# Optimization experiments

Measured on AMD Instinct MI355X. Metric: run time of the kernel, lower is better.

Reference implementation:

```python
import jax, jax.numpy as jnp
import numpy as np

KS = 3
K3 = KS ** 3
NUM_K = 4
KM_ITERS = 10  # fixed Lloyd iterations (original runs to tolerance)


def _unfold3d(xp, d, h, w):
    # xp: [B, C, d+2, h+2, w+2] -> [B, C, d, h, w, 27]; kernel dims flattened as (k1,k2,k3)
    sl = [xp[:, :, i:i + d, j:j + h, l:l + w]
          for i in range(KS) for j in range(KS) for l in range(KS)]
    return jnp.stack(sl, axis=-1)


def _kmeans(pts):
    # pts: [N, C]. Deterministic init with first NUM_K points, fixed Lloyd iterations.
    cent0 = pts[:NUM_K]

    def assign(cent):
        d2 = (jnp.sum(pts * pts, -1, keepdims=True)
              - 2.0 * (pts @ cent.T) + jnp.sum(cent * cent, -1))  # [N, K]
        return jnp.argmin(d2, axis=-1)

    def step(cent, _):
        oh = jax.nn.one_hot(assign(cent), NUM_K, dtype=pts.dtype)  # [N, K]
        cnt = jnp.maximum(oh.sum(0), 1.0)
        cent = (oh.T @ pts) / cnt[:, None]
        return cent, None

    cent, _ = jax.lax.scan(step, cent0, None, length=KM_ITERS)
    return assign(cent), cent


def _mlp3(z, w1, b1, w2, b2, w3, b3):
    z = jax.nn.relu(z @ w1 + b1)
    z = jax.nn.relu(z @ w2 + b2)
    return z @ w3 + b3


def reference(x, proj_w, base_w, gk_w1, gk_b1, gk_w2, gk_b2, gk_w3, gk_b3,
              gb_w1, gb_b1, gb_w2, gb_b2, gb_w3, gb_b3, prelu_a):
    b, c, d, h, w = x.shape
    o = base_w.shape[0]
    n = d * h * w
    x_in = x
    # 1x1x1 input projection (no bias)
    xp = jnp.einsum('oi,bidhw->bodhw', proj_w, x)
    xp = jnp.pad(xp, ((0, 0), (0, 0), (1, 1), (1, 1), (1, 1)))
    patches = _unfold3d(xp, d, h, w)                                # [b,c,d,h,w,27]
    # mean_type 's': mean over kernel dims -> per-voxel channel summary
    x_mean = patches.mean(-1).reshape(b, c, n).transpose(0, 2, 1)   # [b,n,c]
    idx, cent = jax.vmap(_kmeans)(x_mean)                           # [b,n], [b,K,c]
    feat = cent.reshape(b, NUM_K * c)
    # per-cluster dynamic kernel gates in (0,1)
    w_i = jax.nn.sigmoid(_mlp3(feat, gk_w1, gk_b1, gk_w2, gk_b2, gk_w3, gk_b3))
    w_i = w_i.reshape(b, NUM_K, K3).transpose(1, 0, 2)[:, :, None, None, :]  # [K,b,1,1,27]
    weight = (w_i * base_w).reshape(NUM_K, b, o, c * K3)            # [K,b,o,c*27]
    bias = _mlp3(feat, gb_w1, gb_b1, gb_w2, gb_b2, gb_w3, gb_b3)
    bias = bias.reshape(b, NUM_K, o).transpose(1, 0, 2)[..., None]  # [K,b,o,1]
    # im2col: [b, c*27, n] with (c, k) channel-major flattening as in the torch rearrange
    xf = patches.reshape(b, c, n, K3).transpose(0, 1, 3, 2).reshape(b, c * K3, n)
    out = jnp.einsum('kbof,bfn->kbon', weight, xf) + bias           # [K,b,o,n]
    mask = jax.nn.one_hot(idx, NUM_K, dtype=out.dtype)              # [b,n,K]
    out = (out * mask.transpose(2, 0, 1)[:, :, None, :]).sum(0)     # [b,o,n]
    out = out.reshape(b, o, d, h, w)
    out = jnp.where(out >= 0, out, prelu_a * out)                   # PReLU (single param)
    return out + x_in


def setup_inputs():
    key = jax.random.key(0)
    ks = jax.random.split(key, 12)
    B, C, O, D = 1, 64, 64, 40
    inner, inner2 = 128, 64
    fin = C * NUM_K

    def lin(k, i, o_):
        s = 1.0 / np.sqrt(i)
        return jax.random.uniform(k, (i, o_), jnp.float32, -s, s)

    return {
        'x': jax.random.normal(ks[0], (B, C, D, D, D), jnp.float32),
        'proj_w': jax.random.normal(ks[1], (C, C), jnp.float32) / np.sqrt(C),
        'base_w': jax.random.normal(ks[2], (O, C, K3), jnp.float32) / np.sqrt(C * K3),
        'gk_w1': lin(ks[3], fin, inner), 'gk_b1': jnp.zeros((inner,), jnp.float32),
        'gk_w2': lin(ks[4], inner, inner), 'gk_b2': jnp.zeros((inner,), jnp.float32),
        'gk_w3': lin(ks[5], inner, K3 * NUM_K), 'gk_b3': jnp.zeros((K3 * NUM_K,), jnp.float32),
        'gb_w1': lin(ks[6], fin, inner2), 'gb_b1': jnp.zeros((inner2,), jnp.float32),
        'gb_w2': lin(ks[7], inner2, inner2), 'gb_b2': jnp.zeros((inner2,), jnp.float32),
        'gb_w3': lin(ks[8], inner2, O * NUM_K), 'gb_b3': jnp.zeros((O * NUM_K,), jnp.float32),
        'prelu_a': jnp.full((1,), 0.25, jnp.float32),
    }
```

## Files before the change

### kernel.cpp

```cpp
#include <hip/hip_runtime.h>
#include <math.h>

typedef short v8s __attribute__((ext_vector_type(8)));
typedef float v4f __attribute__((ext_vector_type(4)));

#define NVOX 64000
#define NPAD 74088
#define P2   1764
#define GSTR 592704
#define NCPY 32
#define ITST (NCPY*260)

__device__ __forceinline__ unsigned short bf16rne(float f){
  unsigned int u = __float_as_uint(f);
  u += 0x7FFFu + ((u >> 16) & 1u);
  return (unsigned short)(u >> 16);
}

__global__ __launch_bounds__(256) void prep_k(const float* __restrict__ x,
                                              const float* __restrict__ pw,
                                              float* __restrict__ xp,
                                              short* __restrict__ xpt,
                                              const float* __restrict__ bw,
                                              short* __restrict__ bwb,
                                              float* __restrict__ km){
  int tid = threadIdx.x;
  int bid = blockIdx.x;
  if (bid < 1000){
    int m = (bid >> 2) * 256 + tid;
    int quarter = bid & 3;
    float xv[64];
#pragma unroll
    for (int i = 0; i < 64; i++) xv[i] = x[(size_t)i * NVOX + m];
    int d = m / 1600; int r = m - d * 1600; int h = r / 40; int w = r - h * 40;
    int p = ((d + 1) * 42 + (h + 1)) * 42 + (w + 1);
    const float4* pw4 = (const float4*)pw;
    for (int g8 = quarter * 2; g8 < quarter * 2 + 2; g8++){
      v8s pk;
#pragma unroll
      for (int j = 0; j < 8; j++){
        int co = g8 * 8 + j;
        float acc = 0.f;
#pragma unroll
        for (int q = 0; q < 16; q++){
          float4 pv = pw4[co * 16 + q];
          acc = fmaf(pv.x, xv[4*q+0], acc);
          acc = fmaf(pv.y, xv[4*q+1], acc);
          acc = fmaf(pv.z, xv[4*q+2], acc);
          acc = fmaf(pv.w, xv[4*q+3], acc);
        }
        xp[(size_t)co * NVOX + m] = acc;
        pk[j] = (short)bf16rne(acc);
      }
      *(v8s*)(xpt + (size_t)g8 * GSTR + (size_t)p * 8) = pk;
    }
  } else if (bid < 1432){
    int e = (bid - 1000) * 256 + tid;
    int t5 = e >> 12; int rem = e & 4095;
    int o = rem >> 6; int c = rem & 63;
    bwb[e] = (short)bf16rne(bw[(o * 64 + c) * 27 + t5]);
  } else if (bid < 1472){
    v8s z = (v8s){0,0,0,0,0,0,0,0};
    for (int p = (bid - 1432) * 256 + tid; p < NPAD; p += 40 * 256){
      int d = p / P2; int rem = p - d * P2; int h = rem / 42; int w = rem - h * 42;
      if (d == 0 || d == 41 || h == 0 || h == 41 || w == 0 || w == 41){
#pragma unroll
        for (int g = 0; g < 8; g++)
          *(v8s*)(xpt + (size_t)g * GSTR + (size_t)p * 8) = z;
      }
    }
  } else {
    for (int j = (bid - 1472) * 256 + tid; j < 10 * ITST; j += 82 * 256)
      km[j] = 0.f;
  }
}

__global__ __launch_bounds__(256) void boxwh_k(const float* __restrict__ in,
                                               float* __restrict__ out){
  __shared__ float s0[1600], s1[1600];
  size_t base = (size_t)blockIdx.x * 1600;
  int t = threadIdx.x;
  for (int e = t; e < 1600; e += 256) s0[e] = in[base + e];
  __syncthreads();
  for (int e = t; e < 1600; e += 256){
    int w = e % 40;
    float s = s0[e];
    if (w > 0)  s += s0[e - 1];
    if (w < 39) s += s0[e + 1];
    s1[e] = s;
  }
  __syncthreads();
  for (int e = t; e < 1600; e += 256){
    int h = e / 40;
    float s = s1[e];
    if (h > 0)  s += s1[e - 40];
    if (h < 39) s += s1[e + 40];
    out[base + e] = s;
  }
}

__global__ __launch_bounds__(256) void boxdt_k(const float* __restrict__ in,
                                               float* __restrict__ out,
                                               float* __restrict__ acc1){
  __shared__ float tile[64][65];
  __shared__ float s_cent[256];
  __shared__ float s_cc[4];
  __shared__ float s_red[260];
  __shared__ int   s_kb[64];
  int t = threadIdx.x;
  int nb = blockIdx.x * 64;
  int l = t & 63, g = t >> 6;
  {
    int k = t >> 6, c = t & 63;
    s_cent[t] = (in[(size_t)c * NVOX + k] + in[(size_t)c * NVOX + k + 1600]) * (1.f / 27.f);
  }
  for (int j = t; j < 260; j += 256) s_red[j] = 0.f;
  int n = nb + l;
  int d = n / 1600;
  for (int cc = g; cc < 64; cc += 4){
    const float* b = in + (size_t)cc * NVOX + n;
    float s = b[0];
    if (d > 0)  s += b[-1600];
    if (d < 39) s += b[1600];
    tile[cc][l] = s * (1.f / 27.f);
  }
  __syncthreads();
  if (t < 4){
    float s = 0.f;
    for (int c = 0; c < 64; c++){ float v = s_cent[t * 64 + c]; s = fmaf(v, v, s); }
    s_cc[t] = s;
  }
  __syncthreads();
  if (t < 64){
    float d0 = 0.f, d1 = 0.f, d2 = 0.f, d3 = 0.f;
    for (int c = 0; c < 64; c++){
      float v = tile[c][t];
      d0 = fmaf(s_cent[c], v, d0);
      d1 = fmaf(s_cent[64 + c], v, d1);
      d2 = fmaf(s_cent[128 + c], v, d2);
      d3 = fmaf(s_cent[192 + c], v, d3);
    }
    float sc0 = s_cc[0] - 2.f * d0;
    float sc1 = s_cc[1] - 2.f * d1;
    float sc2 = s_cc[2] - 2.f * d2;
    float sc3 = s_cc[3] - 2.f * d3;
    int kb = 0; float bs = sc0;
    if (sc1 < bs){ bs = sc1; kb = 1; }
    if (sc2 < bs){ bs = sc2; kb = 2; }
    if (sc3 < bs){ bs = sc3; kb = 3; }
    s_kb[t] = kb;
  }
  __syncthreads();
  {
    int lane = t & 63, wv = t >> 6;
    float a0 = 0.f, a1 = 0.f, a2 = 0.f, a3 = 0.f;
#pragma unroll
    for (int j = 0; j < 16; j++){
      int p = wv * 16 + j;
      float v = tile[lane][p];
      int kj = s_kb[p];
      a0 += (kj == 0) ? v : 0.f;
      a1 += (kj == 1) ? v : 0.f;
      a2 += (kj == 2) ? v : 0.f;
      a3 += (kj == 3) ? v : 0.f;
    }
    atomicAdd(&s_red[lane], a0);
    atomicAdd(&s_red[64 + lane], a1);
    atomicAdd(&s_red[128 + lane], a2);
    atomicAdd(&s_red[192 + lane], a3);
  }
  if (t < 4){
    float c = 0.f;
    for (int p = 0; p < 64; p++) c += (s_kb[p] == t) ? 1.f : 0.f;
    s_red[256 + t] = c;
  }
  __syncthreads();
  float* kslot = acc1 + (blockIdx.x & (NCPY - 1)) * 260;
  for (int j = t; j < 260; j += 256) atomicAdd(&kslot[j], s_red[j]);
  for (int nn = g; nn < 64; nn += 4)
    out[(size_t)(nb + nn) * 64 + l] = tile[l][nn];
}

__global__ __launch_bounds__(256) void assign_k(const float* __restrict__ xmt,
                                                const float* __restrict__ kin,
                                                float* __restrict__ kout,
                                                int* __restrict__ idx, int mode,
                      const float* __restrict__ w1, const float* __restrict__ b1,
                      const float* __restrict__ w2, const float* __restrict__ b2,
                      const float* __restrict__ w3, const float* __restrict__ b3,
                      const float* __restrict__ u1, const float* __restrict__ c1,
                      const float* __restrict__ u2, const float* __restrict__ c2,
                      const float* __restrict__ u3, const float* __restrict__ c3,
                      float* __restrict__ wi, float* __restrict__ bias){
  __shared__ float s_cent[256];
  __shared__ float s_cc[4];
  __shared__ float s_red[260];
  __shared__ float s_x[256 * 65];
  __shared__ int   s_kb[256];
  __shared__ float s_h1[128], s_h2[128], s_g1[64], s_g2[64];
  int t = threadIdx.x, lane = t & 63, wv = t >> 6;
  int n = blockIdx.x * 256 + t;
  {
    float sum = 0.f, cnt = 0.f;
#pragma unroll
    for (int s = 0; s < NCPY; s++){
      sum += kin[s * 260 + t];
      cnt += kin[s * 260 + 256 + (t >> 6)];
    }
    s_cent[t] = sum / fmaxf(cnt, 1.f);
  }
  for (int j = t; j < 260; j += 256) s_red[j] = 0.f;
  __syncthreads();
  if (t < 4){
    const float4* cc4 = (const float4*)(s_cent + t * 64);
    float s = 0.f;
#pragma unroll
    for (int q = 0; q < 16; q++){
      float4 v = cc4[q];
      s = fmaf(v.x, v.x, s); s = fmaf(v.y, v.y, s);
      s = fmaf(v.z, v.z, s); s = fmaf(v.w, v.w, s);
    }
    s_cc[t] = s;
  }
  __syncthreads();
  const float4* xt = (const float4*)(xmt + (size_t)n * 64);
  float4 xq[16];
#pragma unroll
  for (int q = 0; q < 16; q++) xq[q] = xt[q];
  float d0 = 0.f, d1 = 0.f, d2 = 0.f, d3 = 0.f;
  const float4* c4 = (const float4*)s_cent;
#pragma unroll
  for (int q = 0; q < 16; q++){
    float4 p0 = c4[q], p1 = c4[16 + q], p2 = c4[32 + q], p3 = c4[48 + q];
    d0 = fmaf(p0.x, xq[q].x, d0); d0 = fmaf(p0.y, xq[q].y, d0);
    d0 = fmaf(p0.z, xq[q].z, d0); d0 = fmaf(p0.w, xq[q].w, d0);
    d1 = fmaf(p1.x, xq[q].x, d1); d1 = fmaf(p1.y, xq[q].y, d1);
    d1 = fmaf(p1.z, xq[q].z, d1); d1 = fmaf(p1.w, xq[q].w, d1);
    d2 = fmaf(p2.x, xq[q].x, d2); d2 = fmaf(p2.y, xq[q].y, d2);
    d2 = fmaf(p2.z, xq[q].z, d2); d2 = fmaf(p2.w, xq[q].w, d2);
    d3 = fmaf(p3.x, xq[q].x, d3); d3 = fmaf(p3.y, xq[q].y, d3);
    d3 = fmaf(p3.z, xq[q].z, d3); d3 = fmaf(p3.w, xq[q].w, d3);
  }
  float sc0 = s_cc[0] - 2.f * d0;
  float sc1 = s_cc[1] - 2.f * d1;
  float sc2 = s_cc[2] - 2.f * d2;
  float sc3 = s_cc[3] - 2.f * d3;
  int kb = 0; float bs = sc0;
  if (sc1 < bs){ bs = sc1; kb = 1; }
  if (sc2 < bs){ bs = sc2; kb = 2; }
  if (sc3 < bs){ bs = sc3; kb = 3; }
  if (mode){
    idx[n] = kb;
    if (blockIdx.x == 0){
      __syncthreads();
      if (t < 128){
        float z = b1[t];
        for (int i = 0; i < 256; i++) z = fmaf(s_cent[i], w1[i * 128 + t], z);
        s_h1[t] = fmaxf(z, 0.f);
      }
      if (t < 64){
        float z = c1[t];
        for (int i = 0; i < 256; i++) z = fmaf(s_cent[i], u1[i * 64 + t], z);
        s_g1[t] = fmaxf(z, 0.f);
      }
      __syncthreads();
      if (t < 128){
        float z = b2[t];
        for (int i = 0; i < 128; i++) z = fmaf(s_h1[i], w2[i * 128 + t], z);
        s_h2[t] = fmaxf(z, 0.f);
      }
      if (t < 64){
        float z = c2[t];
        for (int i = 0; i < 64; i++) z = fmaf(s_g1[i], u2[i * 64 + t], z);
        s_g2[t] = fmaxf(z, 0.f);
      }
      __syncthreads();
      if (t < 108){
        float z = b3[t];
        for (int i = 0; i < 128; i++) z = fmaf(s_h2[i], w3[i * 108 + t], z);
        wi[t] = 1.f / (1.f + expf(-z));
      }
      {
        float z = c3[t];
        for (int i = 0; i < 64; i++) z = fmaf(s_g2[i], u3[i * 256 + t], z);
        bias[t] = z;
      }
    }
    return;
  }
  s_kb[t] = kb;
#pragma unroll
  for (int q = 0; q < 16; q++){
    s_x[t * 65 + 4*q + 0] = xq[q].x;
    s_x[t * 65 + 4*q + 1] = xq[q].y;
    s_x[t * 65 + 4*q + 2] = xq[q].z;
    s_x[t * 65 + 4*q + 3] = xq[q].w;
  }
  __syncthreads();
  float a0 = 0.f, a1 = 0.f, a2 = 0.f, a3 = 0.f;
  int rowbase = wv * 64;
#pragma unroll 16
  for (int j = 0; j < 64; j++){
    float v = s_x[(rowbase + j) * 65 + lane];
    int kj = s_kb[rowbase + j];
    a0 += (kj == 0) ? v : 0.f;
    a1 += (kj == 1) ? v : 0.f;
    a2 += (kj == 2) ? v : 0.f;
    a3 += (kj == 3) ? v : 0.f;
  }
  atomicAdd(&s_red[lane], a0);
  atomicAdd(&s_red[64 + lane], a1);
  atomicAdd(&s_red[128 + lane], a2);
  atomicAdd(&s_red[192 + lane], a3);
#pragma unroll
  for (int kk = 0; kk < 4; kk++){
    unsigned long long m = __ballot(kb == kk);
    if (lane == 0) atomicAdd(&s_red[256 + kk], (float)__popcll(m));
  }
  __syncthreads();
  float* kslot = kout + (blockIdx.x & (NCPY - 1)) * 260;
  for (int j = t; j < 260; j += 256) atomicAdd(&kslot[j], s_red[j]);
}

__global__ __launch_bounds__(256) void conv_k(const short* __restrict__ xpt,
                                              const short* __restrict__ bwb,
                                              const float* __restrict__ wi,
                                              const float* __restrict__ bias,
                                              const int* __restrict__ idx,
                                              const float* __restrict__ x,
                                              const float* __restrict__ pa,
                                              float* __restrict__ out){
  static const int POFF[27] = {
    -P2-42-1, -P2-42, -P2-42+1, -P2-1, -P2, -P2+1, -P2+42-1, -P2+42, -P2+42+1,
    -42-1, -42, -42+1, -1, 0, 1, 42-1, 42, 42+1,
    P2-42-1, P2-42, P2-42+1, P2-1, P2, P2+1, P2+42-1, P2+42, P2+42+1 };
  __shared__ float s_wi[108];
  __shared__ float s_bias[256];
  __shared__ float s_acc[64 * 68];
  int tid = threadIdx.x;
  for (int j = tid; j < 108; j += 256) s_wi[j] = wi[j];
  s_bias[tid] = bias[tid];
  __syncthreads();
  int wv = tid >> 6, lane = tid & 63;
  int kc = wv & 1, mh = wv >> 1;
  int col = lane & 15, kg = lane >> 4;
  int vb = blockIdx.x * 64;
  int p4[4], ki4[4];
#pragma unroll
  for (int nt = 0; nt < 4; nt++){
    int v = vb + nt * 16 + col;
    ki4[nt] = idx[v];
    int d = v / 1600; int r = v - d * 1600; int h = r / 40; int w = r - h * 40;
    p4[nt] = ((d + 1) * 42 + (h + 1)) * 42 + (w + 1);
  }
  const short* bg = xpt + (size_t)(kc * 4 + kg) * GSTR;
  const short* bp0 = bg + (size_t)p4[0] * 8;
  const short* bp1 = bg + (size_t)p4[1] * 8;
  const short* bp2 = bg + (size_t)p4[2] * 8;
  const short* bp3 = bg + (size_t)p4[3] * 8;
  int ao0 = (mh * 32 + col) * 64 + kc * 32 + kg * 8;
  int ao1 = ao0 + 16 * 64;
  v4f acc[2][4];
#pragma unroll
  for (int m2 = 0; m2 < 2; m2++)
#pragma unroll
    for (int nt = 0; nt < 4; nt++) acc[m2][nt] = (v4f){0.f, 0.f, 0.f, 0.f};
  v4f zero = {0.f, 0.f, 0.f, 0.f};
#pragma unroll 9
  for (int t = 0; t < 27; t++){
    int po8 = POFF[t] * 8;
    v8s a0 = *(const v8s*)(bwb + t * 4096 + ao0);
    v8s a1 = *(const v8s*)(bwb + t * 4096 + ao1);
    v8s b0 = *(const v8s*)(bp0 + po8);
    v8s b1 = *(const v8s*)(bp1 + po8);
    v8s b2 = *(const v8s*)(bp2 + po8);
    v8s b3 = *(const v8s*)(bp3 + po8);
    float wk0 = s_wi[ki4[0] * 27 + t];
    float wk1 = s_wi[ki4[1] * 27 + t];
    float wk2 = s_wi[ki4[2] * 27 + t];
    float wk3 = s_wi[ki4[3] * 27 + t];
    v4f tp;
    tp = __builtin_amdgcn_mfma_f32_16x16x32_bf16(a0, b0, zero, 0, 0, 0); acc[0][0] += tp * wk0;
    tp = __builtin_amdgcn_mfma_f32_16x16x32_bf16(a1, b0, zero, 0, 0, 0); acc[1][0] += tp * wk0;
    tp = __builtin_amdgcn_mfma_f32_16x16x32_bf16(a0, b1, zero, 0, 0, 0); acc[0][1] += tp * wk1;
    tp = __builtin_amdgcn_mfma_f32_16x16x32_bf16(a1, b1, zero, 0, 0, 0); acc[1][1] += tp * wk1;
    tp = __builtin_amdgcn_mfma_f32_16x16x32_bf16(a0, b2, zero, 0, 0, 0); acc[0][2] += tp * wk2;
    tp = __builtin_amdgcn_mfma_f32_16x16x32_bf16(a1, b2, zero, 0, 0, 0); acc[1][2] += tp * wk2;
    tp = __builtin_amdgcn_mfma_f32_16x16x32_bf16(a0, b3, zero, 0, 0, 0); acc[0][3] += tp * wk3;
    tp = __builtin_amdgcn_mfma_f32_16x16x32_bf16(a1, b3, zero, 0, 0, 0); acc[1][3] += tp * wk3;
  }
  __syncthreads();
  if (kc == 1){
#pragma unroll
    for (int m2 = 0; m2 < 2; m2++)
#pragma unroll
      for (int nt = 0; nt < 4; nt++)
        *(v4f*)(&s_acc[(nt * 16 + col) * 68 + mh * 32 + m2 * 16 + kg * 4]) = acc[m2][nt];
  }
  __syncthreads();
  if (kc == 0){
    float pav = pa[0];
#pragma unroll
    for (int m2 = 0; m2 < 2; m2++){
#pragma unroll
      for (int nt = 0; nt < 4; nt++){
        v4f other = *(const v4f*)(&s_acc[(nt * 16 + col) * 68 + mh * 32 + m2 * 16 + kg * 4]);
        v4f sum = acc[m2][nt] + other;
        int n = vb + nt * 16 + col;
#pragma unroll
        for (int r = 0; r < 4; r++){
          int o = mh * 32 + m2 * 16 + kg * 4 + r;
          float val = sum[r] + s_bias[ki4[nt] * 64 + o];
          val = (val >= 0.f) ? val : pav * val;
          size_t off = (size_t)o * NVOX + n;
          out[off] = val + x[off];
        }
      }
    }
  }
}

extern "C" void kernel_launch(void* const* d_in, const int* in_sizes, int n_in,
                              void* d_out, int out_size, void* d_ws, size_t ws_size,
                              hipStream_t stream){
  const float* x    = (const float*)d_in[0];
  const float* pw   = (const float*)d_in[1];
  const float* bw   = (const float*)d_in[2];
  const float* gkw1 = (const float*)d_in[3];
  const float* gkb1 = (const float*)d_in[4];
  const float* gkw2 = (const float*)d_in[5];
  const float* gkb2 = (const float*)d_in[6];
  const float* gkw3 = (const float*)d_in[7];
  const float* gkb3 = (const float*)d_in[8];
  const float* gbw1 = (const float*)d_in[9];
  const float* gbb1 = (const float*)d_in[10];
  const float* gbw2 = (const float*)d_in[11];
  const float* gbb2 = (const float*)d_in[12];
  const float* gbw3 = (const float*)d_in[13];
  const float* gbb3 = (const float*)d_in[14];
  const float* pa   = (const float*)d_in[15];
  float* outp = (float*)d_out;

  float* ws   = (float*)d_ws;
  float* XP   = ws;
  float* BU2  = ws + 4096000;
  short* XPT  = (short*)(ws + 12288000);
  short* BWB  = XPT + (size_t)NPAD * 64;
  float* KM   = (float*)(BWB + 110592);
  float* WI   = KM + 10 * ITST;
  float* BIAS = WI + 108;
  int*   IDX  = (int*)(BIAS + 256);
  float* XMT  = XP;

  prep_k<<<1554, 256, 0, stream>>>(x, pw, XP, XPT, bw, BWB, KM);
  boxwh_k<<<2560, 256, 0, stream>>>(XP, BU2);
  boxdt_k<<<1000, 256, 0, stream>>>(BU2, XMT, KM);
  for (int it = 1; it <= 10; it++)
    assign_k<<<250, 256, 0, stream>>>(XMT, KM + (it - 1) * ITST,
                                      (it < 10) ? KM + it * ITST : KM, IDX,
                                      (it == 10) ? 1 : 0,
                                      gkw1, gkb1, gkw2, gkb2, gkw3, gkb3,
                                      gbw1, gbb1, gbw2, gbb2, gbw3, gbb3,
                                      WI, BIAS);
  conv_k<<<1000, 256, 0, stream>>>(XPT, BWB, WI, BIAS, IDX, x, pa, outp);
}
```

Measured before the change: 309.6 us.

## Fuse final k-means assignment and gating MLPs into the conv kernel

Drops the tenth assign_k launch (mode=1). Each conv block now rebuilds the centroids from the iteration-9 partial sums, assigns its own 64 voxels, and evaluates both small MLPs into shared memory itself. This removes a kernel launch and the global round trips for idx, wi and bias. In exchange every one of the 1000 conv blocks redundantly runs the serial MLP loops (256x128 weight reads and more) before its convolution starts.

Result: no change. 308.0 us (-0.5%).

```diff
diff --git a/kernel.cpp b/kernel.cpp
--- a/kernel.cpp
+++ b/kernel.cpp
@@ -183,21 +183,12 @@
 
 __global__ __launch_bounds__(256) void assign_k(const float* __restrict__ xmt,
                                                 const float* __restrict__ kin,
-                                                float* __restrict__ kout,
-                                                int* __restrict__ idx, int mode,
-                      const float* __restrict__ w1, const float* __restrict__ b1,
-                      const float* __restrict__ w2, const float* __restrict__ b2,
-                      const float* __restrict__ w3, const float* __restrict__ b3,
-                      const float* __restrict__ u1, const float* __restrict__ c1,
-                      const float* __restrict__ u2, const float* __restrict__ c2,
-                      const float* __restrict__ u3, const float* __restrict__ c3,
-                      float* __restrict__ wi, float* __restrict__ bias){
+                                                float* __restrict__ kout){
   __shared__ float s_cent[256];
   __shared__ float s_cc[4];
   __shared__ float s_red[260];
   __shared__ float s_x[256 * 65];
   __shared__ int   s_kb[256];
-  __shared__ float s_h1[128], s_h2[128], s_g1[64], s_g2[64];
   int t = threadIdx.x, lane = t & 63, wv = t >> 6;
   int n = blockIdx.x * 256 + t;
   {
@@ -249,45 +240,6 @@
   if (sc1 < bs){ bs = sc1; kb = 1; }
   if (sc2 < bs){ bs = sc2; kb = 2; }
   if (sc3 < bs){ bs = sc3; kb = 3; }
-  if (mode){
-    idx[n] = kb;
-    if (blockIdx.x == 0){
-      __syncthreads();
-      if (t < 128){
-        float z = b1[t];
-        for (int i = 0; i < 256; i++) z = fmaf(s_cent[i], w1[i * 128 + t], z);
-        s_h1[t] = fmaxf(z, 0.f);
-      }
-      if (t < 64){
-        float z = c1[t];
-        for (int i = 0; i < 256; i++) z = fmaf(s_cent[i], u1[i * 64 + t], z);
-        s_g1[t] = fmaxf(z, 0.f);
-      }
-      __syncthreads();
-      if (t < 128){
-        float z = b2[t];
-        for (int i = 0; i < 128; i++) z = fmaf(s_h1[i], w2[i * 128 + t], z);
-        s_h2[t] = fmaxf(z, 0.f);
-      }
-      if (t < 64){
-        float z = c2[t];
-        for (int i = 0; i < 64; i++) z = fmaf(s_g1[i], u2[i * 64 + t], z);
-        s_g2[t] = fmaxf(z, 0.f);
-      }
-      __syncthreads();
-      if (t < 108){
-        float z = b3[t];
-        for (int i = 0; i < 128; i++) z = fmaf(s_h2[i], w3[i * 108 + t], z);
-        wi[t] = 1.f / (1.f + expf(-z));
-      }
-      {
-        float z = c3[t];
-        for (int i = 0; i < 64; i++) z = fmaf(s_g2[i], u3[i * 256 + t], z);
-        bias[t] = z;
-      }
-    }
-    return;
-  }
   s_kb[t] = kb;
 #pragma unroll
   for (int q = 0; q < 16; q++){
@@ -324,12 +276,17 @@
 
 __global__ __launch_bounds__(256) void conv_k(const short* __restrict__ xpt,
                                               const short* __restrict__ bwb,
-                                              const float* __restrict__ wi,
-                                              const float* __restrict__ bias,
-                                              const int* __restrict__ idx,
+                                              const float* __restrict__ km,
+                                              const float* __restrict__ xmt,
                                               const float* __restrict__ x,
                                               const float* __restrict__ pa,
-                                              float* __restrict__ out){
+                                              float* __restrict__ out,
+                      const float* __restrict__ w1, const float* __restrict__ b1,
+                      const float* __restrict__ w2, const float* __restrict__ b2,
+                      const float* __restrict__ w3, const float* __restrict__ b3,
+                      const float* __restrict__ u1, const float* __restrict__ c1,
+                      const float* __restrict__ u2, const float* __restrict__ c2,
+                      const float* __restrict__ u3, const float* __restrict__ c3){
   static const int POFF[27] = {
     -P2-42-1, -P2-42, -P2-42+1, -P2-1, -P2, -P2+1, -P2+42-1, -P2+42, -P2+42+1,
     -42-1, -42, -42+1, -1, 0, 1, 42-1, 42, 42+1,
@@ -337,19 +294,104 @@
   __shared__ float s_wi[108];
   __shared__ float s_bias[256];
   __shared__ float s_acc[64 * 68];
+  __shared__ float s_cent[256];
+  __shared__ float s_cc[4];
+  __shared__ int   s_kb[64];
+  __shared__ float s_h1[128], s_h2[128], s_g1[64], s_g2[64];
   int tid = threadIdx.x;
-  for (int j = tid; j < 108; j += 256) s_wi[j] = wi[j];
-  s_bias[tid] = bias[tid];
+  int vb = blockIdx.x * 64;
+  {
+    float sum = 0.f, cnt = 0.f;
+#pragma unroll
+    for (int s = 0; s < NCPY; s++){
+      sum += km[s * 260 + tid];
+      cnt += km[s * 260 + 256 + (tid >> 6)];
+    }
+    s_cent[tid] = sum / fmaxf(cnt, 1.f);
+  }
+  __syncthreads();
+  if (tid < 4){
+    const float4* cc4 = (const float4*)(s_cent + tid * 64);
+    float s = 0.f;
+#pragma unroll
+    for (int q = 0; q < 16; q++){
+      float4 v = cc4[q];
+      s = fmaf(v.x, v.x, s); s = fmaf(v.y, v.y, s);
+      s = fmaf(v.z, v.z, s); s = fmaf(v.w, v.w, s);
+    }
+    s_cc[tid] = s;
+  }
+  __syncthreads();
+  if (tid < 64){
+    const float4* xt = (const float4*)(xmt + (size_t)(vb + tid) * 64);
+    float4 xq[16];
+#pragma unroll
+    for (int q = 0; q < 16; q++) xq[q] = xt[q];
+    float d0 = 0.f, d1 = 0.f, d2 = 0.f, d3 = 0.f;
+    const float4* c4 = (const float4*)s_cent;
+#pragma unroll
+    for (int q = 0; q < 16; q++){
+      float4 p0 = c4[q], p1 = c4[16 + q], p2 = c4[32 + q], p3 = c4[48 + q];
+      d0 = fmaf(p0.x, xq[q].x, d0); d0 = fmaf(p0.y, xq[q].y, d0);
+      d0 = fmaf(p0.z, xq[q].z, d0); d0 = fmaf(p0.w, xq[q].w, d0);
+      d1 = fmaf(p1.x, xq[q].x, d1); d1 = fmaf(p1.y, xq[q].y, d1);
+      d1 = fmaf(p1.z, xq[q].z, d1); d1 = fmaf(p1.w, xq[q].w, d1);
+      d2 = fmaf(p2.x, xq[q].x, d2); d2 = fmaf(p2.y, xq[q].y, d2);
+      d2 = fmaf(p2.z, xq[q].z, d2); d2 = fmaf(p2.w, xq[q].w, d2);
+      d3 = fmaf(p3.x, xq[q].x, d3); d3 = fmaf(p3.y, xq[q].y, d3);
+      d3 = fmaf(p3.z, xq[q].z, d3); d3 = fmaf(p3.w, xq[q].w, d3);
+    }
+    float sc0 = s_cc[0] - 2.f * d0;
+    float sc1 = s_cc[1] - 2.f * d1;
+    float sc2 = s_cc[2] - 2.f * d2;
+    float sc3 = s_cc[3] - 2.f * d3;
+    int kb = 0; float bs = sc0;
+    if (sc1 < bs){ bs = sc1; kb = 1; }
+    if (sc2 < bs){ bs = sc2; kb = 2; }
+    if (sc3 < bs){ bs = sc3; kb = 3; }
+    s_kb[tid] = kb;
+  }
+  if (tid < 128){
+    float z = b1[tid];
+    for (int i = 0; i < 256; i++) z = fmaf(s_cent[i], w1[i * 128 + tid], z);
+    s_h1[tid] = fmaxf(z, 0.f);
+  }
+  if (tid < 64){
+    float z = c1[tid];
+    for (int i = 0; i < 256; i++) z = fmaf(s_cent[i], u1[i * 64 + tid], z);
+    s_g1[tid] = fmaxf(z, 0.f);
+  }
+  __syncthreads();
+  if (tid < 128){
+    float z = b2[tid];
+    for (int i = 0; i < 128; i++) z = fmaf(s_h1[i], w2[i * 128 + tid], z);
+    s_h2[tid] = fmaxf(z, 0.f);
+  }
+  if (tid < 64){
+    float z = c2[tid];
+    for (int i = 0; i < 64; i++) z = fmaf(s_g1[i], u2[i * 64 + tid], z);
+    s_g2[tid] = fmaxf(z, 0.f);
+  }
+  __syncthreads();
+  if (tid < 108){
+    float z = b3[tid];
+    for (int i = 0; i < 128; i++) z = fmaf(s_h2[i], w3[i * 108 + tid], z);
+    s_wi[tid] = 1.f / (1.f + expf(-z));
+  }
+  {
+    float z = c3[tid];
+    for (int i = 0; i < 64; i++) z = fmaf(s_g2[i], u3[i * 256 + tid], z);
+    s_bias[tid] = z;
+  }
   __syncthreads();
   int wv = tid >> 6, lane = tid & 63;
   int kc = wv & 1, mh = wv >> 1;
   int col = lane & 15, kg = lane >> 4;
-  int vb = blockIdx.x * 64;
   int p4[4], ki4[4];
 #pragma unroll
   for (int nt = 0; nt < 4; nt++){
     int v = vb + nt * 16 + col;
-    ki4[nt] = idx[v];
+    ki4[nt] = s_kb[nt * 16 + col];
     int d = v / 1600; int r = v - d * 1600; int h = r / 40; int w = r - h * 40;
     p4[nt] = ((d + 1) * 42 + (h + 1)) * 42 + (w + 1);
   }
@@ -447,20 +489,14 @@
   short* XPT  = (short*)(ws + 12288000);
   short* BWB  = XPT + (size_t)NPAD * 64;
   float* KM   = (float*)(BWB + 110592);
-  float* WI   = KM + 10 * ITST;
-  float* BIAS = WI + 108;
-  int*   IDX  = (int*)(BIAS + 256);
   float* XMT  = XP;
 
   prep_k<<<1554, 256, 0, stream>>>(x, pw, XP, XPT, bw, BWB, KM);
   boxwh_k<<<2560, 256, 0, stream>>>(XP, BU2);
   boxdt_k<<<1000, 256, 0, stream>>>(BU2, XMT, KM);
-  for (int it = 1; it <= 10; it++)
-    assign_k<<<250, 256, 0, stream>>>(XMT, KM + (it - 1) * ITST,
-                                      (it < 10) ? KM + it * ITST : KM, IDX,
-                                      (it == 10) ? 1 : 0,
-                                      gkw1, gkb1, gkw2, gkb2, gkw3, gkb3,
-                                      gbw1, gbb1, gbw2, gbb2, gbw3, gbb3,
-                                      WI, BIAS);
-  conv_k<<<1000, 256, 0, stream>>>(XPT, BWB, WI, BIAS, IDX, x, pa, outp);
-}
+  for (int it = 1; it <= 9; it++)
+    assign_k<<<250, 256, 0, stream>>>(XMT, KM + (it - 1) * ITST, KM + it * ITST);
+  conv_k<<<1000, 256, 0, stream>>>(XPT, BWB, KM + 9 * ITST, XMT, x, pa, outp,
+                                   gkw1, gkb1, gkw2, gkb2, gkw3, gkb3,
+                                   gbw1, gbb1, gbw2, gbb2, gbw3, gbb3);
+}
```
